# Optimization experiments

Hardware: AMD Instinct MI355X
Metric: run time of the kernel (lower is better)

The kernel has to match this reference:

```python
import jax, jax.numpy as jnp
import numpy as np

B, S, N, D = 4, 8, 1024, 512
PROJ_DIM = 512
HEADS = 4
EPSILON = 0.01


def pose_encoding(p):
    # p: [B,S,N,d]; faithful to PoseEncoding.__call__
    n, d = p.shape[-2], p.shape[-1]
    sin_d = d // 2 if d % 2 == 0 else (d - 1) // 2 + 1
    cos_d = d // 2 if d % 2 == 0 else (d - 1) // 2
    idx = jnp.arange(n, dtype=p.dtype)[:, None]
    ks = jnp.arange(sin_d, dtype=p.dtype)[None, :]
    kc = jnp.arange(cos_d, dtype=p.dtype)[None, :]
    sin_ape = jnp.sin(idx / (1000.0 * (2.0 * ks / d) + 0.01))  # [N, sin_d]
    cos_ape = jnp.cos(idx / (1000.0 * (2.0 * kc / d) + 0.01))  # [N, cos_d]
    pe = jnp.zeros((n, d), dtype=p.dtype)
    pe = pe.at[:, 0::2].set(sin_ape).at[:, 1::2].set(cos_ape)
    return p + pe


def setup_inputs() -> dict:
    key = jax.random.key(0)
    ks = jax.random.split(key, 5)
    x = jax.random.normal(ks[0], (B, S, N, D), dtype=jnp.float32)
    Wqkv = jax.random.normal(ks[1], (HEADS, D, 3 * D), dtype=jnp.float32) * 0.02
    bqkv = jax.random.normal(ks[2], (HEADS, 3 * D), dtype=jnp.float32) * 0.02
    Wp = jax.random.normal(ks[3], (HEADS, D, PROJ_DIM), dtype=jnp.float32) * 0.02
    bp = jax.random.normal(ks[4], (HEADS, PROJ_DIM), dtype=jnp.float32) * 0.02
    return {"x": x, "Wqkv": Wqkv, "bqkv": bqkv, "Wp": Wp, "bp": bp}


def reference(x, Wqkv, bqkv, Wp, bp):
    b, s, n, d = x.shape
    heads = Wqkv.shape[0]
    pred_proj = None
    proj = None
    for h in range(heads):  # small fixed loop over structurally distinct heads
        qkv = jax.nn.selu(jnp.einsum('bsnd,de->bsne', x, Wqkv[h]) + bqkv[h])
        qkv = qkv.reshape(b, s, n, 3, d)
        q, k, v = qkv[..., 0, :], qkv[..., 1, :], qkv[..., 2, :]
        # non-standard ordering: scale QK^T, multiply by V, THEN softmax
        qkT = jnp.einsum('bsnd,bsmd->bsnm', q, k) / d  # [B,S,N,N]
        att = jax.nn.softmax(jnp.einsum('bsnm,bsmd->bsnd', qkT, v), axis=-1)
        proj = jax.nn.gelu(jnp.einsum('bsnd,dp->bsnp', att, Wp[h]) + bp[h],
                           approximate=False)
        if pred_proj is None:
            pred_proj = proj
        else:
            proj = proj + EPSILON * pred_proj  # pred_proj stays = head-0 proj (as in source)
    return pose_encoding(proj)
```

## Files before the change

### kernel.cpp

```cpp
#include <hip/hip_runtime.h>
#include <hip/hip_bf16.h>
#include <math.h>

typedef unsigned short u16;
typedef unsigned int   u32;
typedef __bf16  v8bf  __attribute__((ext_vector_type(8)));
typedef float   v4f   __attribute__((ext_vector_type(4)));

#define EPS_H 0.01f

typedef const __attribute__((address_space(1))) void* gas_t;
typedef __attribute__((address_space(3))) void* las_t;
#define GL2LDS(g,l) __builtin_amdgcn_global_load_lds((gas_t)(const void*)(g), (las_t)(void*)(l), 16, 0, 0)

#define VMW8()   asm volatile("s_waitcnt vmcnt(8)" ::: "memory")
#define VMW0()   asm volatile("s_waitcnt vmcnt(0)" ::: "memory")
#define BAR()    __builtin_amdgcn_s_barrier()
#define SCHED0() __builtin_amdgcn_sched_barrier(0)

__device__ __forceinline__ u16 f2bf(float f) {
    __bf16 h = (__bf16)f;
    return *reinterpret_cast<u16*>(&h);
}
__device__ __forceinline__ float bfs(u16 v) { return __uint_as_float(((u32)v) << 16); }
__device__ __forceinline__ float selu_f(float x) {
    const float sc = 1.0507009873554805f, al = 1.6732632423543772f;
    return x > 0.f ? sc * x : sc * al * (__expf(x) - 1.0f);
}
__device__ __forceinline__ float gelu_f(float x) {
    return 0.5f * x * (1.f + erff(x * 0.7071067811865476f));
}
__device__ __forceinline__ float pe_val(int n, int j) {
    float t = 1000.0f * ((float)(j & ~1) * (1.0f / 512.0f)) + 0.01f;
    float a = (float)n / t;
    return (j & 1) ? cosf(a) : sinf(a);
}

__device__ __forceinline__ v8bf lfrag(const u16* base, int row, int lane) {
    int g = (lane >> 4) ^ ((row >> 1) & 3);
    return *(const v8bf*)((const char*)base + row * 64 + g * 16);
}

__device__ __forceinline__ void stage2(const u16* g, size_t gstride, u16* lds, int wave, int lane) {
    const int l2 = lane >> 2;
    #pragma unroll
    for (int i = 0; i < 4; ++i) {
        const int ib  = wave * 4 + i;
        const int sub = ib >> 3;
        const int rl  = (ib & 7) * 16 + l2;
        const int gs  = (lane & 3) ^ ((rl >> 1) & 3);
        GL2LDS((const char*)(g + (size_t)rl * gstride + sub * 32) + gs * 16,
               (char*)lds + ib * 1024);
    }
}

#define COMPUTE_TILE(Abuf, Bbuf)                                                   \
    {                                                                              \
        const u16* A0 = &(Abuf)[0];    const u16* A1 = &(Abuf)[4096];              \
        const u16* B0 = &(Bbuf)[0];    const u16* B1 = &(Bbuf)[4096];              \
        v8bf b0[4], b1[4];                                                         \
        _Pragma("unroll")                                                          \
        for (int fc = 0; fc < 4; ++fc) {                                           \
            const int brow = wn * 64 + fc * 16 + (lane & 15);                      \
            b0[fc] = lfrag(B0, brow, lane);                                        \
            b1[fc] = lfrag(B1, brow, lane);                                        \
        }                                                                          \
        __builtin_amdgcn_s_setprio(1);                                             \
        _Pragma("unroll")                                                          \
        for (int fr = 0; fr < 4; ++fr) {                                           \
            const int arow = wm * 64 + fr * 16 + (lane & 15);                      \
            v8bf a0 = lfrag(A0, arow, lane);                                       \
            v8bf a1 = lfrag(A1, arow, lane);                                       \
            _Pragma("unroll")                                                      \
            for (int fc = 0; fc < 4; ++fc) {                                       \
                acc[fr][fc] = __builtin_amdgcn_mfma_f32_16x16x32_bf16(a0, b0[fc], acc[fr][fc], 0, 0, 0); \
                acc[fr][fc] = __builtin_amdgcn_mfma_f32_16x16x32_bf16(a1, b1[fc], acc[fr][fc], 0, 0, 0); \
            }                                                                      \
        }                                                                          \
        __builtin_amdgcn_s_setprio(0);                                             \
    }

__global__ __launch_bounds__(256)
void k_prep(const float* __restrict__ x, u16* __restrict__ xbf, float* __restrict__ pe,
            const float* __restrict__ Wqkv, u16* __restrict__ WqT,
            const float* __restrict__ Wp, u16* __restrict__ WpT)
{
    __shared__ float t[32][33];
    const int b = blockIdx.x, tid = threadIdx.x;
    if (b < 8192) {
        const size_t i = ((size_t)b * 256 + tid) * 8;
        float4 a = *(const float4*)&x[i];
        float4 c = *(const float4*)&x[i + 4];
        ushort4 o0, o1;
        o0.x = f2bf(a.x); o0.y = f2bf(a.y); o0.z = f2bf(a.z); o0.w = f2bf(a.w);
        o1.x = f2bf(c.x); o1.y = f2bf(c.y); o1.z = f2bf(c.z); o1.w = f2bf(c.w);
        *(ushort4*)&xbf[i] = o0;
        *(ushort4*)&xbf[i + 4] = o1;
        return;
    }
    if (b < 10240) {
        int idx = (b - 8192) * 256 + tid;
        pe[idx] = pe_val(idx >> 9, idx & 511);
        return;
    }
    const float* src; u16* dst; int rows, cols, bx, by;
    if (b < 11776) {
        int l = b - 10240, hh = l / 768, rem = l % 768;
        bx = rem % 48; by = rem / 48;
        src = Wqkv + (size_t)(hh ? 3 : 0) * 786432; dst = WqT + (size_t)hh * 786432;
        rows = 512; cols = 1536;
    } else {
        int l = b - 11776, hh = l / 256, rem = l % 256;
        bx = rem % 16; by = rem / 16;
        src = Wp + (size_t)(hh ? 3 : 0) * 262144; dst = WpT + (size_t)hh * 262144;
        rows = 512; cols = 512;
    }
    const int c0 = bx * 32, r0 = by * 32;
    #pragma unroll
    for (int i = 0; i < 4; ++i) {
        int idx = tid + i * 256;
        int rr = idx >> 5, cc = idx & 31;
        t[rr][cc] = src[(size_t)(r0 + rr) * cols + c0 + cc];
    }
    __syncthreads();
    #pragma unroll
    for (int i = 0; i < 4; ++i) {
        int idx = tid + i * 256;
        int rr = idx >> 5, cc = idx & 31;
        dst[(size_t)(c0 + rr) * rows + r0 + cc] = f2bf(t[cc][rr]);
    }
}

__global__ __launch_bounds__(256, 1)
void k1_qkv(const u16* __restrict__ xbf, const u16* __restrict__ WT,
            const float* __restrict__ bias, u16* __restrict__ q,
            u16* __restrict__ kT, u16* __restrict__ vT)
{
    __shared__ u16 Als[2][8192];
    __shared__ u16 Bls[2][8192];
    const int tid = threadIdx.x, lane = tid & 63, wave = tid >> 6;
    const int orig = blockIdx.x + blockIdx.y * 12;
    const int swz  = (orig & 7) * 192 + (orig >> 3);
    const int col0 = (swz % 12) * 128, row0 = (swz / 12) * 128;
    const int wm = wave >> 1, wn = wave & 1;
    const u16* Ab = xbf + (size_t)row0 * 512;
    const u16* Bb = WT + (size_t)col0 * 512;
    v4f acc[4][4] = {};

    stage2(Ab,      512, &Als[0][0], wave, lane);
    stage2(Bb,      512, &Bls[0][0], wave, lane);
    stage2(Ab + 64, 512, &Als[1][0], wave, lane);
    stage2(Bb + 64, 512, &Bls[1][0], wave, lane);
    for (int t = 0; t < 8; ++t) {
        const int c = t & 1;
        if (t < 7) VMW8(); else VMW0();
        BAR(); SCHED0();
        COMPUTE_TILE(Als[c], Bls[c]);
        BAR(); SCHED0();
        if (t + 2 < 8) {
            const int k0 = (t + 2) * 64;
            stage2(Ab + k0, 512, &Als[c][0], wave, lane);
            stage2(Bb + k0, 512, &Bls[c][0], wave, lane);
        }
    }

    const int region = col0 >> 9;
    #pragma unroll
    for (int fn = 0; fn < 4; ++fn) {
        const int c = col0 + wn * 64 + fn * 16 + (lane & 15);
        const float bc = bias[c];
        #pragma unroll
        for (int fm = 0; fm < 4; ++fm) {
            const int rb = row0 + wm * 64 + fm * 16 + ((lane >> 4) << 2);
            float v0 = selu_f(acc[fm][fn][0] + bc);
            float v1 = selu_f(acc[fm][fn][1] + bc);
            float v2 = selu_f(acc[fm][fn][2] + bc);
            float v3 = selu_f(acc[fm][fn][3] + bc);
            if (region == 0) {
                q[(size_t)(rb + 0) * 512 + c] = f2bf(v0);
                q[(size_t)(rb + 1) * 512 + c] = f2bf(v1);
                q[(size_t)(rb + 2) * 512 + c] = f2bf(v2);
                q[(size_t)(rb + 3) * 512 + c] = f2bf(v3);
            } else {
                ushort4 st; st.x = f2bf(v0); st.y = f2bf(v1); st.z = f2bf(v2); st.w = f2bf(v3);
                const int seq = rb >> 10, n = rb & 1023;
                u16* dst = (region == 1) ? kT : vT;
                const int cc = c - ((region == 1) ? 512 : 1024);
                *(ushort4*)&dst[(size_t)seq * 524288 + (size_t)cc * 1024 + n] = st;
            }
        }
    }
}

__global__ __launch_bounds__(256, 1)
void k2_ktv(const u16* __restrict__ kT, const u16* __restrict__ vT, u16* __restrict__ Mt)
{
    __shared__ u16 Als[2][8192];
    __shared__ u16 Bls[2][8192];
    const int tid = threadIdx.x, lane = tid & 63, wave = tid >> 6;
    const int d0 = blockIdx.x * 128, p0 = blockIdx.y * 128, seq = blockIdx.z;
    const u16* Ab = kT + (size_t)seq * 524288 + (size_t)d0 * 1024;
    const u16* Bb = vT + (size_t)seq * 524288 + (size_t)p0 * 1024;
    const int wm = wave >> 1, wn = wave & 1;
    v4f acc[4][4] = {};

    stage2(Ab,      1024, &Als[0][0], wave, lane);
    stage2(Bb,      1024, &Bls[0][0], wave, lane);
    stage2(Ab + 64, 1024, &Als[1][0], wave, lane);
    stage2(Bb + 64, 1024, &Bls[1][0], wave, lane);
    for (int t = 0; t < 16; ++t) {
        const int c = t & 1;
        if (t < 15) VMW8(); else VMW0();
        BAR(); SCHED0();
        COMPUTE_TILE(Als[c], Bls[c]);
        BAR(); SCHED0();
        if (t + 2 < 16) {
            const int m0 = (t + 2) * 64;
            stage2(Ab + m0, 1024, &Als[c][0], wave, lane);
            stage2(Bb + m0, 1024, &Bls[c][0], wave, lane);
        }
    }

    #pragma unroll
    for (int fn = 0; fn < 4; ++fn) {
        const int p = p0 + wn * 64 + fn * 16 + (lane & 15);
        #pragma unroll
        for (int fm = 0; fm < 4; ++fm) {
            const int d = d0 + wm * 64 + fm * 16 + ((lane >> 4) << 2);
            ushort4 st;
            st.x = f2bf(acc[fm][fn][0] * (1.f / 512.f));
            st.y = f2bf(acc[fm][fn][1] * (1.f / 512.f));
            st.z = f2bf(acc[fm][fn][2] * (1.f / 512.f));
            st.w = f2bf(acc[fm][fn][3] * (1.f / 512.f));
            *(ushort4*)&Mt[(size_t)seq * 262144 + (size_t)p * 512 + d] = st;
        }
    }
}

__global__ __launch_bounds__(256, 1)
void k3a_s(const u16* __restrict__ q, const u16* __restrict__ Mt, u16* __restrict__ S)
{
    __shared__ u16 Als[2][8192];
    __shared__ u16 Bls[2][8192];
    const int tid = threadIdx.x, lane = tid & 63, wave = tid >> 6;
    const int orig = blockIdx.x + blockIdx.y * 4;
    const int swz  = (orig & 7) * 64 + (orig >> 3);
    const int p0 = (swz % 4) * 128, row0 = (swz / 4) * 128;
    const int seq = row0 >> 10;
    const u16* Ab = q + (size_t)row0 * 512;
    const u16* Bb = Mt + (size_t)seq * 262144 + (size_t)p0 * 512;
    const int wm = wave >> 1, wn = wave & 1;
    v4f acc[4][4] = {};

    stage2(Ab,      512, &Als[0][0], wave, lane);
    stage2(Bb,      512, &Bls[0][0], wave, lane);
    stage2(Ab + 64, 512, &Als[1][0], wave, lane);
    stage2(Bb + 64, 512, &Bls[1][0], wave, lane);
    for (int t = 0; t < 8; ++t) {
        const int c = t & 1;
        if (t < 7) VMW8(); else VMW0();
        BAR(); SCHED0();
        COMPUTE_TILE(Als[c], Bls[c]);
        BAR(); SCHED0();
        if (t + 2 < 8) {
            const int k0 = (t + 2) * 64;
            stage2(Ab + k0, 512, &Als[c][0], wave, lane);
            stage2(Bb + k0, 512, &Bls[c][0], wave, lane);
        }
    }

    #pragma unroll
    for (int fn = 0; fn < 4; ++fn) {
        const int c = p0 + wn * 64 + fn * 16 + (lane & 15);
        #pragma unroll
        for (int fm = 0; fm < 4; ++fm) {
            const int rb = row0 + wm * 64 + fm * 16 + ((lane >> 4) << 2);
            S[(size_t)(rb + 0) * 512 + c] = f2bf(acc[fm][fn][0]);
            S[(size_t)(rb + 1) * 512 + c] = f2bf(acc[fm][fn][1]);
            S[(size_t)(rb + 2) * 512 + c] = f2bf(acc[fm][fn][2]);
            S[(size_t)(rb + 3) * 512 + c] = f2bf(acc[fm][fn][3]);
        }
    }
}

__global__ __launch_bounds__(256)
void k3b_sm(u16* __restrict__ S)
{
    const int row  = blockIdx.x * 4 + (threadIdx.x >> 6);
    const int lane = threadIdx.x & 63;
    u16* rp = S + (size_t)row * 512 + lane * 8;
    ushort4 u0 = *(const ushort4*)rp;
    ushort4 u1 = *(const ushort4*)(rp + 4);
    float f[8] = {bfs(u0.x), bfs(u0.y), bfs(u0.z), bfs(u0.w),
                  bfs(u1.x), bfs(u1.y), bfs(u1.z), bfs(u1.w)};
    float m = f[0];
    #pragma unroll
    for (int j = 1; j < 8; ++j) m = fmaxf(m, f[j]);
    #pragma unroll
    for (int off = 32; off > 0; off >>= 1) m = fmaxf(m, __shfl_xor(m, off));
    float s = 0.f;
    #pragma unroll
    for (int j = 0; j < 8; ++j) { f[j] = __expf(f[j] - m); s += f[j]; }
    #pragma unroll
    for (int off = 32; off > 0; off >>= 1) s += __shfl_xor(s, off);
    const float inv = 1.0f / s;
    ushort4 o0, o1;
    o0.x = f2bf(f[0] * inv); o0.y = f2bf(f[1] * inv);
    o0.z = f2bf(f[2] * inv); o0.w = f2bf(f[3] * inv);
    o1.x = f2bf(f[4] * inv); o1.y = f2bf(f[5] * inv);
    o1.z = f2bf(f[6] * inv); o1.w = f2bf(f[7] * inv);
    *(ushort4*)rp = o0;
    *(ushort4*)(rp + 4) = o1;
}

__global__ __launch_bounds__(256, 1)
void k3c_proj(const u16* __restrict__ att, const u16* __restrict__ WpT,
              const float* __restrict__ bp, const float* __restrict__ pe,
              float* __restrict__ out, const int mode, const int rowbase)
{
    __shared__ u16 Als[2][8192];
    __shared__ u16 Bls[2][8192];
    const int tid = threadIdx.x, lane = tid & 63, wave = tid >> 6;
    const int orig = blockIdx.x + blockIdx.y * 4;
    const int swz  = (orig & 7) * 64 + (orig >> 3);
    const int e0 = (swz % 4) * 128, row0 = (swz / 4) * 128;
    const u16* Ab = att + (size_t)row0 * 512;
    const u16* Bb = WpT + (size_t)e0 * 512;
    const int wm = wave >> 1, wn = wave & 1;
    v4f acc[4][4] = {};

    stage2(Ab,      512, &Als[0][0], wave, lane);
    stage2(Bb,      512, &Bls[0][0], wave, lane);
    stage2(Ab + 64, 512, &Als[1][0], wave, lane);
    stage2(Bb + 64, 512, &Bls[1][0], wave, lane);
    for (int t = 0; t < 8; ++t) {
        const int c = t & 1;
        if (t < 7) VMW8(); else VMW0();
        BAR(); SCHED0();
        COMPUTE_TILE(Als[c], Bls[c]);
        BAR(); SCHED0();
        if (t + 2 < 8) {
            const int k0 = (t + 2) * 64;
            stage2(Ab + k0, 512, &Als[c][0], wave, lane);
            stage2(Bb + k0, 512, &Bls[c][0], wave, lane);
        }
    }

    #pragma unroll
    for (int fn = 0; fn < 4; ++fn) {
        const int e = e0 + wn * 64 + fn * 16 + (lane & 15);
        const float be = bp[e];
        #pragma unroll
        for (int fm = 0; fm < 4; ++fm) {
            const int rb = row0 + wm * 64 + fm * 16 + ((lane >> 4) << 2);
            #pragma unroll
            for (int j = 0; j < 4; ++j) {
                const int r = rowbase + rb + j;
                const float g = gelu_f(acc[fm][fn][j] + be);
                const size_t o = (size_t)r * 512 + e;
                if (mode == 0) out[o] = g;
                else           out[o] = g + EPS_H * out[o] + pe[(r & 1023) * 512 + e];
            }
        }
    }
}

extern "C" void kernel_launch(void* const* d_in, const int* in_sizes, int n_in,
                              void* d_out, int out_size, void* d_ws, size_t ws_size,
                              hipStream_t stream)
{
    const float* x    = (const float*)d_in[0];
    const float* Wqkv = (const float*)d_in[1];
    const float* bqkv = (const float*)d_in[2];
    const float* Wp   = (const float*)d_in[3];
    const float* bp   = (const float*)d_in[4];
    float* out = (float*)d_out;

    char* ws = (char*)d_ws;
    u16*   xbf = (u16*)(ws);
    u16*   q   = (u16*)(ws + 33554432);
    u16*   kT  = (u16*)(ws + 50331648);
    u16*   vT  = (u16*)(ws + 67108864);
    u16*   Mt  = (u16*)(ws + 83886080);
    u16*   WqT = (u16*)(ws + 92274688);
    u16*   WpT = (u16*)(ws + 95420416);
    float* pe  = (float*)(ws + 96468992);
    u16*   S   = kT;

    k_prep<<<12288, 256, 0, stream>>>(x, xbf, pe, Wqkv, WqT, Wp, WpT);
    for (int p = 0; p < 2; ++p) {
        const int h = p ? 3 : 0;
        for (int ck = 0; ck < 2; ++ck) {
            const u16* xc = xbf + (size_t)ck * 16384 * 512;
            k1_qkv<<<dim3(12, 128), 256, 0, stream>>>(xc, WqT + (size_t)p * 786432,
                                                      bqkv + (size_t)h * 1536, q, kT, vT);
            k2_ktv<<<dim3(4, 4, 16), 256, 0, stream>>>(kT, vT, Mt);
            k3a_s<<<dim3(4, 128), 256, 0, stream>>>(q, Mt, S);
            k3b_sm<<<4096, 256, 0, stream>>>(S);
            k3c_proj<<<dim3(4, 128), 256, 0, stream>>>(S, WpT + (size_t)p * 262144,
                                                       bp + (size_t)h * 512, pe, out, p, ck * 16384);
        }
    }
}
```

Baseline: 436.9 us.

## Replace QKV GEMM with 256x256-tile 8-wave kernel and split Q computation

The 128x128 QKV GEMM kernel is replaced by a 512-thread kernel that computes 256x256 output tiles. It stages A and B in half-K chunks into 128KB of dynamic LDS with an XOR swizzle, and interleaves loads with four compute phases per k-step, raising MFMA priority during compute. Q for the full batch is now computed in one launch per head, and K/V per chunk in a separate launch, which needs a larger workspace for Q. The goal is more data reuse per LDS load and better load/compute overlap, at the cost of one block per CU, more registers and an extra launch.

```diff
diff --git a/kernel.cpp b/kernel.cpp
--- a/kernel.cpp
+++ b/kernel.cpp
@@ -14,6 +14,8 @@
 #define GL2LDS(g,l) __builtin_amdgcn_global_load_lds((gas_t)(const void*)(g), (las_t)(void*)(l), 16, 0, 0)
 
 #define VMW8()   asm volatile("s_waitcnt vmcnt(8)" ::: "memory")
+#define VMW6()   asm volatile("s_waitcnt vmcnt(6)" ::: "memory")
+#define VMW4()   asm volatile("s_waitcnt vmcnt(4)" ::: "memory")
 #define VMW0()   asm volatile("s_waitcnt vmcnt(0)" ::: "memory")
 #define BAR()    __builtin_amdgcn_s_barrier()
 #define SCHED0() __builtin_amdgcn_sched_barrier(0)
@@ -131,62 +133,100 @@
     }
 }
 
-__global__ __launch_bounds__(256, 1)
-void k1_qkv(const u16* __restrict__ xbf, const u16* __restrict__ WT,
+__global__ __launch_bounds__(512, 1)
+void k1_8ph(const u16* __restrict__ xsrc, const u16* __restrict__ WT,
             const float* __restrict__ bias, u16* __restrict__ q,
-            u16* __restrict__ kT, u16* __restrict__ vT)
-{
-    __shared__ u16 Als[2][8192];
-    __shared__ u16 Bls[2][8192];
+            u16* __restrict__ kT, u16* __restrict__ vT, const int mode)
+{
+    extern __shared__ u16 lds[];
     const int tid = threadIdx.x, lane = tid & 63, wave = tid >> 6;
-    const int orig = blockIdx.x + blockIdx.y * 12;
-    const int swz  = (orig & 7) * 192 + (orig >> 3);
-    const int col0 = (swz % 12) * 128, row0 = (swz / 12) * 128;
-    const int wm = wave >> 1, wn = wave & 1;
-    const u16* Ab = xbf + (size_t)row0 * 512;
-    const u16* Bb = WT + (size_t)col0 * 512;
-    v4f acc[4][4] = {};
-
-    stage2(Ab,      512, &Als[0][0], wave, lane);
-    stage2(Bb,      512, &Bls[0][0], wave, lane);
-    stage2(Ab + 64, 512, &Als[1][0], wave, lane);
-    stage2(Bb + 64, 512, &Bls[1][0], wave, lane);
+    const int wm = wave >> 2, wn = wave & 3;
+    const int b = blockIdx.x;
+    const int swz = (b & 7) * 32 + (b >> 3);
+    int rt, col0;
+    if (mode == 0) { rt = swz >> 1; col0 = (swz & 1) * 256; }
+    else           { rt = swz >> 2; col0 = 512 + (swz & 3) * 256; }
+    const int row0 = rt * 256;
+    const u16* Ag = xsrc + (size_t)row0 * 512;
+    const u16* Bg = WT + (size_t)col0 * 512;
+    v4f acc[8][4] = {};
+
+    auto stg = [&](const u16* g, int kt, int kh, int isB) {
+        char* base = (char*)lds + isB * 65536 + (kt & 1) * 32768 + kh * 8192;
+        #pragma unroll
+        for (int i = 0; i < 2; ++i) {
+            const int ib = wave * 2 + i;
+            const int rh = ib >> 3, ch = ib & 7;
+            const int rl = ch * 16 + (lane >> 2);
+            const int row = rh * 128 + rl;
+            const int gs = (lane & 3) ^ ((rl >> 1) & 3);
+            GL2LDS((const char*)(g + (size_t)row * 512 + kt * 64 + kh * 32) + gs * 16,
+                   base + rh * 16384 + ch * 1024);
+        }
+    };
+
+    stg(Ag, 0, 0, 0); stg(Bg, 0, 0, 1); stg(Ag, 0, 1, 0); stg(Bg, 0, 1, 1);
+
     for (int t = 0; t < 8; ++t) {
-        const int c = t & 1;
-        if (t < 7) VMW8(); else VMW0();
-        BAR(); SCHED0();
-        COMPUTE_TILE(Als[c], Bls[c]);
-        BAR(); SCHED0();
-        if (t + 2 < 8) {
-            const int k0 = (t + 2) * 64;
-            stage2(Ab + k0, 512, &Als[c][0], wave, lane);
-            stage2(Bb + k0, 512, &Bls[c][0], wave, lane);
-        }
-    }
-
-    const int region = col0 >> 9;
-    #pragma unroll
-    for (int fn = 0; fn < 4; ++fn) {
-        const int c = col0 + wn * 64 + fn * 16 + (lane & 15);
+        const u16* Asl = lds + (t & 1) * 16384;
+        const u16* Bsl = lds + 32768 + (t & 1) * 16384;
+        #pragma unroll
+        for (int ph = 0; ph < 4; ++ph) {
+            const int kh = ph >> 1, mh = ph & 1;
+            if (t < 7) {
+                if      (ph == 0) stg(Ag, t + 1, 0, 0);
+                else if (ph == 1) stg(Bg, t + 1, 0, 1);
+                else if (ph == 2) stg(Ag, t + 1, 1, 0);
+                else              stg(Bg, t + 1, 1, 1);
+            }
+            if (ph == 0)      { if (t < 7) VMW6(); else VMW4(); }
+            else if (ph == 2) { if (t < 7) VMW6(); else VMW0(); }
+            BAR(); SCHED0();
+            {
+                const u16* Asub = Asl + wm * 8192 + kh * 4096;
+                const u16* Bsub = Bsl + (wn >> 1) * 8192 + kh * 4096;
+                v8bf af[4], bf[4];
+                #pragma unroll
+                for (int i = 0; i < 4; ++i)
+                    af[i] = lfrag(Asub, (mh * 4 + i) * 16 + (lane & 15), lane);
+                #pragma unroll
+                for (int n = 0; n < 4; ++n)
+                    bf[n] = lfrag(Bsub, (wn & 1) * 64 + n * 16 + (lane & 15), lane);
+                __builtin_amdgcn_s_setprio(1);
+                #pragma unroll
+                for (int i = 0; i < 4; ++i)
+                    #pragma unroll
+                    for (int n = 0; n < 4; ++n)
+                        acc[mh * 4 + i][n] =
+                            __builtin_amdgcn_mfma_f32_16x16x32_bf16(af[i], bf[n], acc[mh * 4 + i][n], 0, 0, 0);
+                __builtin_amdgcn_s_setprio(0);
+            }
+            BAR(); SCHED0();
+        }
+    }
+
+    #pragma unroll
+    for (int n = 0; n < 4; ++n) {
+        const int c = col0 + wn * 64 + n * 16 + (lane & 15);
         const float bc = bias[c];
         #pragma unroll
-        for (int fm = 0; fm < 4; ++fm) {
-            const int rb = row0 + wm * 64 + fm * 16 + ((lane >> 4) << 2);
-            float v0 = selu_f(acc[fm][fn][0] + bc);
-            float v1 = selu_f(acc[fm][fn][1] + bc);
-            float v2 = selu_f(acc[fm][fn][2] + bc);
-            float v3 = selu_f(acc[fm][fn][3] + bc);
-            if (region == 0) {
+        for (int m = 0; m < 8; ++m) {
+            const int rb = row0 + wm * 128 + m * 16 + ((lane >> 4) << 2);
+            float v0 = selu_f(acc[m][n][0] + bc);
+            float v1 = selu_f(acc[m][n][1] + bc);
+            float v2 = selu_f(acc[m][n][2] + bc);
+            float v3 = selu_f(acc[m][n][3] + bc);
+            if (mode == 0) {
                 q[(size_t)(rb + 0) * 512 + c] = f2bf(v0);
                 q[(size_t)(rb + 1) * 512 + c] = f2bf(v1);
                 q[(size_t)(rb + 2) * 512 + c] = f2bf(v2);
                 q[(size_t)(rb + 3) * 512 + c] = f2bf(v3);
             } else {
                 ushort4 st; st.x = f2bf(v0); st.y = f2bf(v1); st.z = f2bf(v2); st.w = f2bf(v3);
-                const int seq = rb >> 10, n = rb & 1023;
-                u16* dst = (region == 1) ? kT : vT;
-                const int cc = c - ((region == 1) ? 512 : 1024);
-                *(ushort4*)&dst[(size_t)seq * 524288 + (size_t)cc * 1024 + n] = st;
+                const int seq = rb >> 10, nn = rb & 1023;
+                u16* dst = (c < 1024) ? kT : vT;
+                const int cc = c - ((c < 1024) ? 512 : 1024);
+                *(ushort4*)&dst[(size_t)seq * 524288 + (size_t)cc * 1024 + nn] = st;
             }
         }
     }
@@ -356,10 +396,10 @@
             #pragma unroll
             for (int j = 0; j < 4; ++j) {
                 const int r = rowbase + rb + j;
-                const float g = gelu_f(acc[fm][fn][j] + be);
+                const float g2 = gelu_f(acc[fm][fn][j] + be);
                 const size_t o = (size_t)r * 512 + e;
-                if (mode == 0) out[o] = g;
-                else           out[o] = g + EPS_H * out[o] + pe[(r & 1023) * 512 + e];
+                if (mode == 0) out[o] = g2;
+                else           out[o] = g2 + EPS_H * out[o] + pe[(r & 1023) * 512 + e];
             }
         }
     }
@@ -379,23 +419,29 @@
     char* ws = (char*)d_ws;
     u16*   xbf = (u16*)(ws);
     u16*   q   = (u16*)(ws + 33554432);
-    u16*   kT  = (u16*)(ws + 50331648);
-    u16*   vT  = (u16*)(ws + 67108864);
-    u16*   Mt  = (u16*)(ws + 83886080);
-    u16*   WqT = (u16*)(ws + 92274688);
-    u16*   WpT = (u16*)(ws + 95420416);
-    float* pe  = (float*)(ws + 96468992);
+    u16*   kT  = (u16*)(ws + 67108864);
+    u16*   vT  = (u16*)(ws + 83886080);
+    u16*   Mt  = (u16*)(ws + 100663296);
+    u16*   WqT = (u16*)(ws + 109051904);
+    u16*   WpT = (u16*)(ws + 112197632);
+    float* pe  = (float*)(ws + 113246208);
     u16*   S   = kT;
+
+    (void)hipFuncSetAttribute((const void*)k1_8ph,
+                              hipFuncAttributeMaxDynamicSharedMemorySize, 131072);
 
     k_prep<<<12288, 256, 0, stream>>>(x, xbf, pe, Wqkv, WqT, Wp, WpT);
     for (int p = 0; p < 2; ++p) {
         const int h = p ? 3 : 0;
+        k1_8ph<<<256, 512, 131072, stream>>>(xbf, WqT + (size_t)p * 786432,
+                                             bqkv + (size_t)h * 1536, q, nullptr, nullptr, 0);
         for (int ck = 0; ck < 2; ++ck) {
             const u16* xc = xbf + (size_t)ck * 16384 * 512;
-            k1_qkv<<<dim3(12, 128), 256, 0, stream>>>(xc, WqT + (size_t)p * 786432,
-                                                      bqkv + (size_t)h * 1536, q, kT, vT);
+            const u16* qc = q   + (size_t)ck * 16384 * 512;
+            k1_8ph<<<256, 512, 131072, stream>>>(xc, WqT + (size_t)p * 786432,
+                                                 bqkv + (size_t)h * 1536, nullptr, kT, vT, 1);
             k2_ktv<<<dim3(4, 4, 16), 256, 0, stream>>>(kT, vT, Mt);
-            k3a_s<<<dim3(4, 128), 256, 0, stream>>>(q, Mt, S);
+            k3a_s<<<dim3(4, 128), 256, 0, stream>>>(qc, Mt, S);
             k3b_sm<<<4096, 256, 0, stream>>>(S);
             k3c_proj<<<dim3(4, 128), 256, 0, stream>>>(S, WpT + (size_t)p * 262144,
                                                        bp + (size_t)h * 512, pe, out, p, ck * 16384);
```

Result: slower. 447.2 us (+2.3%).
